# Kernel tuning notes

Measured on AMD Instinct MI355X. Metric: run time of the kernel, lower is better.

Reference implementation:

```python
import jax, jax.numpy as jnp
import numpy as np

N = 20000
F_IN = 128
HID = 128
HEADS = 8
NCLS = 18
NEG_SLOPE = 0.2


def setup_inputs() -> dict:
    key = jax.random.key(0)
    ks = jax.random.split(key, 12)
    x = jax.random.normal(ks[0], (N, F_IN), dtype=jnp.float32)
    edge_index = jax.random.randint(ks[1], (2, 200000), 0, N)
    sc1 = 1.0 / np.sqrt(F_IN)
    sc2 = 1.0 / np.sqrt(HEADS * HID)
    W1 = jax.random.normal(ks[2], (F_IN, HEADS * HID), dtype=jnp.float32) * sc1
    a1_src = jax.random.normal(ks[3], (HEADS, HID), dtype=jnp.float32) * sc1
    a1_dst = jax.random.normal(ks[4], (HEADS, HID), dtype=jnp.float32) * sc1
    b1 = jnp.zeros((HEADS * HID,), dtype=jnp.float32)
    W2 = jax.random.normal(ks[5], (HEADS * HID, NCLS), dtype=jnp.float32) * sc2
    a2_src = jax.random.normal(ks[6], (1, NCLS), dtype=jnp.float32) * sc2
    a2_dst = jax.random.normal(ks[7], (1, NCLS), dtype=jnp.float32) * sc2
    b2 = jnp.zeros((NCLS,), dtype=jnp.float32)
    return {"x": x, "edge_index": edge_index, "W1": W1, "a1_src": a1_src,
            "a1_dst": a1_dst, "b1": b1, "W2": W2, "a2_src": a2_src,
            "a2_dst": a2_dst, "b2": b2}


def gat_conv(x, src, dst, W, a_src, a_dst, b, heads, out_ch):
    n = x.shape[0]
    h = (x @ W).reshape(n, heads, out_ch)              # [N,H,C]
    alpha_s = jnp.sum(h * a_src, axis=-1)              # [N,H]
    alpha_d = jnp.sum(h * a_dst, axis=-1)              # [N,H]
    e = jax.nn.leaky_relu(alpha_s[src] + alpha_d[dst], NEG_SLOPE)  # [E,H]
    # per-destination softmax (segment softmax)
    m = jax.ops.segment_max(e, dst, num_segments=n)
    e = jnp.exp(e - m[dst])
    z = jax.ops.segment_sum(e, dst, num_segments=n)
    alpha = e / (z[dst] + 1e-16)                       # [E,H]
    out = jax.ops.segment_sum(alpha[:, :, None] * h[src], dst, num_segments=n)
    return out.reshape(n, heads * out_ch) + b


def reference(x, edge_index, W1, a1_src, a1_dst, b1, W2, a2_src, a2_dst, b2):
    n = x.shape[0]
    # PyG GATConv adds self-loops by default
    loops = jnp.arange(n, dtype=edge_index.dtype)
    src = jnp.concatenate([edge_index[0], loops])
    dst = jnp.concatenate([edge_index[1], loops])
    h = gat_conv(x, src, dst, W1, a1_src, a1_dst, b1, HEADS, HID)
    h = jax.nn.relu(h)
    # F.dropout(training=self.training) is identity in eval mode
    out = gat_conv(h, src, dst, W2, a2_src, a2_dst, b2, 1, NCLS)
    return out
```

## Files before the change

kernel.cpp:

```cpp
#include <hip/hip_runtime.h>
#include <math.h>

#define FIN 128
#define NH 8
#define HC 128
#define HD (NH*HC)
#define NC 18
#define NW2 32
#define NEG 0.2f

typedef __attribute__((ext_vector_type(8))) short bf16x8;
typedef __attribute__((ext_vector_type(4))) float f32x4;

__device__ __forceinline__ float lrelu(float v){ return v > 0.f ? v : NEG*v; }

__device__ __forceinline__ unsigned short f2b(float f){
  unsigned u = __float_as_uint(f);
  unsigned r = (u + 0x7fffu + ((u >> 16) & 1u)) >> 16;
  return (unsigned short)r;
}
__device__ __forceinline__ float b2f_lo(unsigned u){ return __uint_as_float(u << 16); }
__device__ __forceinline__ float b2f_hi(unsigned u){ return __uint_as_float(u & 0xffff0000u); }

__device__ __forceinline__ void acc8(float* a, float w, uint4 r){
  a[0] += w*b2f_lo(r.x); a[1] += w*b2f_hi(r.x);
  a[2] += w*b2f_lo(r.y); a[3] += w*b2f_hi(r.y);
  a[4] += w*b2f_lo(r.z); a[5] += w*b2f_hi(r.z);
  a[6] += w*b2f_lo(r.w); a[7] += w*b2f_hi(r.w);
}

__global__ __launch_bounds__(1024) void scan_k(const int* __restrict__ deg, int N,
                                               int* __restrict__ off, int* __restrict__ cursor){
  __shared__ int wsum[16];
  int t = threadIdx.x, lane = t & 63, wid = t >> 6;
  int PER = (N + 1023) >> 10;
  int base = t * PER;
  int sum = 0;
  for (int i = 0; i < PER; ++i) {
    int idx = base + i;
    if (idx < N) sum += deg[idx];
  }
  int x = sum;
  #pragma unroll
  for (int o = 1; o < 64; o <<= 1) {
    int y = __shfl_up(x, o, 64);
    if (lane >= o) x += y;
  }
  if (lane == 63) wsum[wid] = x;
  __syncthreads();
  if (wid == 0 && lane < 16) {
    int wv = wsum[lane];
    #pragma unroll
    for (int o = 1; o < 16; o <<= 1) {
      int y = __shfl_up(wv, o, 16);
      if (lane >= o) wv += y;
    }
    wsum[lane] = wv;
  }
  __syncthreads();
  int carry = x - sum + (wid > 0 ? wsum[wid-1] : 0);
  int run = carry;
  for (int i = 0; i < PER; ++i) {
    int idx = base + i;
    if (idx < N) {
      off[idx] = run; cursor[idx] = run;
      run += deg[idx];
    }
  }
  if (base < N && base + PER >= N) off[N] = run;
}

__global__ void scatter_k(const int* __restrict__ ei, int E0, int N,
                          int* __restrict__ cursor, int* __restrict__ csr){
  int e = blockIdx.x*256 + threadIdx.x;
  int tot = E0 + N;
  if (e >= tot) return;
  int src, dst;
  if (e < E0) { src = ei[e]; dst = ei[E0 + e]; }
  else        { src = e - E0; dst = src; }
  int p = atomicAdd(&cursor[dst], 1);
  csr[p] = src;
}

__global__ __launch_bounds__(256) void prep_k(const float* __restrict__ x,
    const float* __restrict__ W1, const float* __restrict__ W2,
    const float* __restrict__ a1s, const float* __restrict__ a1d,
    const int* __restrict__ ei,
    unsigned short* __restrict__ xb, unsigned short* __restrict__ w1t,
    unsigned short* __restrict__ w2t, unsigned short* __restrict__ ut_g,
    int* __restrict__ deg,
    int total8, int bX, int E0, int N){
  __shared__ unsigned short sT[FIN][64+2];
  int b = blockIdx.x, t = threadIdx.x;
  if (b < bX) {
    int i = b*256 + t;
    if (i < total8) {
      const float4* p = (const float4*)x + (size_t)i*2;
      float4 a = p[0], c = p[1];
      uint4 o;
      o.x = (unsigned)f2b(a.x) | ((unsigned)f2b(a.y) << 16);
      o.y = (unsigned)f2b(a.z) | ((unsigned)f2b(a.w) << 16);
      o.z = (unsigned)f2b(c.x) | ((unsigned)f2b(c.y) << 16);
      o.w = (unsigned)f2b(c.z) | ((unsigned)f2b(c.w) << 16);
      ((uint4*)xb)[i] = o;
    }
    return;
  }
  b -= bX;
  if (b < 16) {
    int n0 = b * 64;
    #pragma unroll
    for (int i = 0; i < 32; ++i) {
      int idx = i*256 + t;
      int k = idx >> 6, nl = idx & 63;
      sT[k][nl] = f2b(W1[(size_t)k*HD + n0 + nl]);
    }
    __syncthreads();
    #pragma unroll
    for (int i = 0; i < 16; ++i) {
      int nl = i*4 + (t >> 6);
      int kp = t & 63;
      unsigned u = (unsigned)sT[2*kp][nl] | ((unsigned)sT[2*kp+1][nl] << 16);
      *(unsigned*)&w1t[(size_t)(n0+nl)*FIN + 2*kp] = u;
    }
    return;
  }
  b -= 16;
  if (b < (NW2*HD)/256) {
    int idx = b*256 + t;
    int n = idx >> 10, k = idx & 1023;
    w2t[idx] = (n < NC) ? f2b(W2[(size_t)k*NC + n]) : (unsigned short)0;
    return;
  }
  b -= (NW2*HD)/256;
  if (b < 16) {
    int c = b;
    int h = c >> 1;
    const float* av = (c & 1) ? &a1d[h*HC] : &a1s[h*HC];
    if (t < FIN) {
      const float4* wr = (const float4*)&W1[(size_t)t*HD + h*HC];
      const float4* ap = (const float4*)av;
      float s = 0.f;
      #pragma unroll 8
      for (int q = 0; q < HC/4; ++q) {
        float4 w4 = wr[q], a4 = ap[q];
        s += w4.x*a4.x + w4.y*a4.y + w4.z*a4.z + w4.w*a4.w;
      }
      ut_g[c*FIN + t] = f2b(s);
    }
    return;
  }
  b -= 16;
  {
    int e = b*256 + t;
    int tot = E0 + N;
    if (e >= tot) return;
    int dst = (e < E0) ? ei[E0 + e] : (e - E0);
    atomicAdd(&deg[dst], 1);
  }
}

__global__ __launch_bounds__(256) void gemm1_mfma_k(const unsigned short* __restrict__ xb,
    const unsigned short* __restrict__ w1t, const unsigned short* __restrict__ ut_g,
    unsigned short* __restrict__ g1b, float* __restrict__ as1, float* __restrict__ ad1,
    int N){
  __shared__ unsigned short sA[128][136];
  __shared__ unsigned short sB[128][136];
  __shared__ unsigned short sU[16][136];
  int t = threadIdx.x, lane = t & 63, wid = t >> 6;
  int bm = blockIdx.x * 128;
  int head = blockIdx.y;
  int bn = head * 128;
  #pragma unroll
  for (int i = 0; i < 2; ++i) {
    int idx = i*256 + t;
    int row = idx >> 2, seg = idx & 3;
    int gm = bm + row;
    uint4 a0,a1,a2,a3;
    if (gm < N) {
      const uint4* gp = (const uint4*)(xb + (size_t)gm*FIN + seg*32);
      a0 = gp[0]; a1 = gp[1]; a2 = gp[2]; a3 = gp[3];
    } else {
      a0 = a1 = a2 = a3 = make_uint4(0,0,0,0);
    }
    uint4* lp = (uint4*)&sA[row][seg*32];
    lp[0]=a0; lp[1]=a1; lp[2]=a2; lp[3]=a3;
  }
  #pragma unroll
  for (int i = 0; i < 2; ++i) {
    int idx = i*256 + t;
    int row = idx >> 2, seg = idx & 3;
    const uint4* gp = (const uint4*)(w1t + (size_t)(bn + row)*FIN + seg*32);
    uint4* lp = (uint4*)&sB[row][seg*32];
    lp[0]=gp[0]; lp[1]=gp[1]; lp[2]=gp[2]; lp[3]=gp[3];
  }
  bool alpha_blk = (head == 0);
  if (alpha_blk) {
    int row = t >> 4, seg = t & 15;
    *(uint4*)&sU[row][seg*8] = *(const uint4*)&ut_g[row*FIN + seg*8];
  }
  __syncthreads();
  int wr = wid >> 1, wc = wid & 1;
  int lr = lane & 15, kb = lane >> 4;
  bool alpha_wave = alpha_blk && (wc == 0);
  f32x4 acc[4][4];
  f32x4 accA[4];
  #pragma unroll
  for (int mi = 0; mi < 4; ++mi) {
    f32x4 z = {0.f,0.f,0.f,0.f};
    accA[mi] = z;
    #pragma unroll
    for (int ni = 0; ni < 4; ++ni) acc[mi][ni] = z;
  }
  #pragma unroll
  for (int ks = 0; ks < 4; ++ks) {
    int ko = ks*32 + kb*8;
    bf16x8 a[4], b[4];
    #pragma unroll
    for (int mi = 0; mi < 4; ++mi)
      a[mi] = *(const bf16x8*)&sA[wr*64 + mi*16 + lr][ko];
    #pragma unroll
    for (int ni = 0; ni < 4; ++ni)
      b[ni] = *(const bf16x8*)&sB[wc*64 + ni*16 + lr][ko];
    #pragma unroll
    for (int mi = 0; mi < 4; ++mi)
      #pragma unroll
      for (int ni = 0; ni < 4; ++ni)
        acc[mi][ni] = __builtin_amdgcn_mfma_f32_16x16x32_bf16(a[mi], b[ni], acc[mi][ni], 0, 0, 0);
    if (alpha_wave) {
      bf16x8 ub = *(const bf16x8*)&sU[lr][ko];
      #pragma unroll
      for (int mi = 0; mi < 4; ++mi)
        accA[mi] = __builtin_amdgcn_mfma_f32_16x16x32_bf16(a[mi], ub, accA[mi], 0, 0, 0);
    }
  }
  __syncthreads();

  if (alpha_wave) {
    int hcol = lr >> 1;
    float* dst0 = (lr & 1) ? ad1 : as1;
    #pragma unroll
    for (int mi = 0; mi < 4; ++mi)
      #pragma unroll
      for (int r = 0; r < 4; ++r) {
        int row = bm + wr*64 + mi*16 + kb*4 + r;
        if (row < N) dst0[(size_t)row*NH + hcol] = accA[mi][r];
      }
  }
  #pragma unroll
  for (int mi = 0; mi < 4; ++mi)
    #pragma unroll
    for (int ni = 0; ni < 4; ++ni) {
      int col = wc*64 + ni*16 + lr;
      #pragma unroll
      for (int r = 0; r < 4; ++r)
        sA[wr*64 + mi*16 + kb*4 + r][col] = f2b(acc[mi][ni][r]);
    }
  __syncthreads();
  {
    int row = t >> 1, half = t & 1;
    int grow = bm + row;
    if (grow < N) {
      uint4* dst = (uint4*)(g1b + (size_t)grow*HD + bn + half*64);
      const uint4* src = (const uint4*)&sA[row][half*64];
      #pragma unroll
      for (int q = 0; q < 8; ++q) dst[q] = src[q];
    }
  }
}

__global__ __launch_bounds__(256) void attn1_k(const unsigned short* __restrict__ g1b,
    const float* __restrict__ as1, const float* __restrict__ ad1,
    const int* __restrict__ off, const int* __restrict__ csr,
    const float* __restrict__ b1, const unsigned short* __restrict__ w2t,
    const float* __restrict__ a2s_g, const float* __restrict__ a2d_g,
    float* __restrict__ g2, float* __restrict__ as2, float* __restrict__ ad2, int N){
  __shared__ unsigned short tile[16][1032];
  __shared__ float red[4][4][32];
  int t = threadIdx.x, lane = t & 63, wid = t >> 6;
  int d = blockIdx.x*4 + wid;
  bool active = (d < N);
  int beg = 0, deg = 0;
  int hg = lane >> 3;
  float adg = 0.f;
  if (active) {
    beg = off[d]; deg = off[d+1] - beg;
    adg = ad1[d*NH + hg];
  }
  float m = -1e30f, z = 0.f;
  float acc[16];
  #pragma unroll
  for (int i = 0; i < 16; ++i) acc[i] = 0.f;

  int j = 0;
  for (; j + 4 <= deg; j += 4) {
    int s0 = csr[beg+j+0], s1 = csr[beg+j+1], s2 = csr[beg+j+2], s3 = csr[beg+j+3];
    const uint4* p0 = (const uint4*)(g1b + (size_t)s0*HD) + lane*2;
    const uint4* p1 = (const uint4*)(g1b + (size_t)s1*HD) + lane*2;
    const uint4* p2 = (const uint4*)(g1b + (size_t)s2*HD) + lane*2;
    const uint4* p3 = (const uint4*)(g1b + (size_t)s3*HD) + lane*2;
    uint4 r00 = p0[0], r01 = p0[1];
    uint4 r10 = p1[0], r11 = p1[1];
    uint4 r20 = p2[0], r21 = p2[1];
    uint4 r30 = p3[0], r31 = p3[1];
    float e0 = lrelu(as1[s0*NH+hg] + adg);
    float e1 = lrelu(as1[s1*NH+hg] + adg);
    float e2 = lrelu(as1[s2*NH+hg] + adg);
    float e3 = lrelu(as1[s3*NH+hg] + adg);
    float em = fmaxf(fmaxf(e0,e1), fmaxf(e2,e3));
    if (em > m) {
      float sc = __expf(m - em);
      z *= sc;
      #pragma unroll
      for (int i = 0; i < 16; ++i) acc[i] *= sc;
      m = em;
    }
    float w0 = __expf(e0 - m), w1 = __expf(e1 - m);
    float w2 = __expf(e2 - m), w3 = __expf(e3 - m);
    z += w0 + w1 + w2 + w3;
    acc8(acc, w0, r00); acc8(acc+8, w0, r01);
    acc8(acc, w1, r10); acc8(acc+8, w1, r11);
    acc8(acc, w2, r20); acc8(acc+8, w2, r21);
    acc8(acc, w3, r30); acc8(acc+8, w3, r31);
  }
  for (; j < deg; ++j) {
    int s = csr[beg+j];
    const uint4* p = (const uint4*)(g1b + (size_t)s*HD) + lane*2;
    uint4 r0 = p[0], r1 = p[1];
    float e = lrelu(as1[s*NH+hg] + adg);
    if (e > m) {
      float sc = __expf(m - e);
      z *= sc;
      #pragma unroll
      for (int i = 0; i < 16; ++i) acc[i] *= sc;
      m = e;
    }
    float w = __expf(e - m);
    z += w;
    acc8(acc, w, r0); acc8(acc+8, w, r1);
  }

  {
    float zinv = 1.f / (z + 1e-16f);
    int cb = lane*16;
    uint o[8];
    #pragma unroll
    for (int q = 0; q < 4; ++q) {
      float4 bv = *(const float4*)&b1[cb + q*4];
      float v0 = fmaxf(acc[q*4+0]*zinv + bv.x, 0.f);
      float v1 = fmaxf(acc[q*4+1]*zinv + bv.y, 0.f);
      float v2 = fmaxf(acc[q*4+2]*zinv + bv.z, 0.f);
      float v3 = fmaxf(acc[q*4+3]*zinv + bv.w, 0.f);
      o[q*2+0] = (unsigned)f2b(v0) | ((unsigned)f2b(v1) << 16);
      o[q*2+1] = (unsigned)f2b(v2) | ((unsigned)f2b(v3) << 16);
    }
    uint4* lp = (uint4*)&tile[wid][lane*16];
    lp[0] = make_uint4(o[0], o[1], o[2], o[3]);
    lp[1] = make_uint4(o[4], o[5], o[6], o[7]);
  }
  __syncthreads();

  {
    int lr = lane & 15, kb = lane >> 4;
    f32x4 c0 = {0.f,0.f,0.f,0.f}, c1 = {0.f,0.f,0.f,0.f};
    #pragma unroll
    for (int ks = 0; ks < 8; ++ks) {
      int k = wid*256 + ks*32 + kb*8;
      bf16x8 af = *(const bf16x8*)&tile[lr][k];
      bf16x8 b0 = *(const bf16x8*)&w2t[(size_t)lr*HD + k];
      bf16x8 b1f = *(const bf16x8*)&w2t[(size_t)(16+lr)*HD + k];
      c0 = __builtin_amdgcn_mfma_f32_16x16x32_bf16(af, b0, c0, 0,0,0);
      c1 = __builtin_amdgcn_mfma_f32_16x16x32_bf16(af, b1f, c1, 0,0,0);
    }
    if (kb == 0) {
      #pragma unroll
      for (int r = 0; r < 4; ++r) {
        red[wid][r][lr]      = c0[r];
        red[wid][r][16 + lr] = c1[r];
      }
    }
  }
  __syncthreads();
  if (t < 128) {
    int dl = t >> 5, c = t & 31;
    float v = red[0][dl][c] + red[1][dl][c] + red[2][dl][c] + red[3][dl][c];
    float vs = (c < NC) ? v * a2s_g[c] : 0.f;
    float vd = (c < NC) ? v * a2d_g[c] : 0.f;
    #pragma unroll
    for (int o = 1; o < 32; o <<= 1) {
      vs += __shfl_xor(vs, o, 32);
      vd += __shfl_xor(vd, o, 32);
    }
    int dg = blockIdx.x*4 + dl;
    if (dg < N) {
      if (c < NC) g2[(size_t)dg*NC + c] = v;
      if (c == 0) { as2[dg] = vs; ad2[dg] = vd; }
    }
  }
}

__global__ __launch_bounds__(256) void attn2_k(const float* __restrict__ g2,
    const float* __restrict__ as2, const float* __restrict__ ad2,
    const int* __restrict__ off, const int* __restrict__ csr,
    const float* __restrict__ b2, float* __restrict__ out, int N){
  int t = threadIdx.x, lane = t & 63, wid = t >> 6;
  int d = blockIdx.x*4 + wid;
  if (d >= N) return;
  int beg = off[d], deg = off[d+1] - beg;
  float adv = ad2[d];
  int g = lane / 18;
  int c = lane - g*18;
  float m = -1e30f, z = 0.f, acc = 0.f;
  if (g < 3) {
    int j = g;
    for (; j + 3 < deg; j += 6) {
      int sa = csr[beg+j], sb = csr[beg+j+3];
      float va = g2[(size_t)sa*NC + c];
      float vb = g2[(size_t)sb*NC + c];
      float ea = lrelu(as2[sa] + adv);
      float eb = lrelu(as2[sb] + adv);
      float em = fmaxf(ea, eb);
      if (em > m) { float sc = __expf(m - em); z *= sc; acc *= sc; m = em; }
      float wa = __expf(ea - m), wb = __expf(eb - m);
      z += wa + wb;
      acc += wa*va + wb*vb;
    }
    for (; j < deg; j += 3) {
      int s = csr[beg+j];
      float v = g2[(size_t)s*NC + c];
      float e = lrelu(as2[s] + adv);
      if (e > m) { float sc = __expf(m - e); z *= sc; acc *= sc; m = e; }
      float w = __expf(e - m);
      z += w;
      acc += w*v;
    }
  }
  float m0 = __shfl(m, 0),  m1 = __shfl(m, 18), m2 = __shfl(m, 36);
  float M  = fmaxf(m0, fmaxf(m1, m2));
  float e0 = __expf(m0 - M), e1 = __expf(m1 - M), e2 = __expf(m2 - M);
  float z0 = __shfl(z, 0),  z1 = __shfl(z, 18), z2 = __shfl(z, 36);
  int cl = (lane < NC) ? lane : 0;
  float a0 = __shfl(acc, cl), a1 = __shfl(acc, cl+18), a2 = __shfl(acc, cl+36);
  if (lane < NC) {
    float Z = z0*e0 + z1*e1 + z2*e2;
    float A = a0*e0 + a1*e1 + a2*e2;
    out[(size_t)d*NC + lane] = A / (Z + 1e-16f) + b2[lane];
  }
}

extern "C" void kernel_launch(void* const* d_in, const int* in_sizes, int n_in,
                              void* d_out, int out_size, void* d_ws, size_t ws_size,
                              hipStream_t stream){
  const float* x   = (const float*)d_in[0];
  const int*   ei  = (const int*)d_in[1];
  const float* W1  = (const float*)d_in[2];
  const float* a1s = (const float*)d_in[3];
  const float* a1d = (const float*)d_in[4];
  const float* b1  = (const float*)d_in[5];
  const float* W2  = (const float*)d_in[6];
  const float* a2s = (const float*)d_in[7];
  const float* a2d = (const float*)d_in[8];
  const float* b2  = (const float*)d_in[9];
  float* out = (float*)d_out;
  int N  = in_sizes[0] / FIN;
  int E0 = in_sizes[1] / 2;
  int Etot = E0 + N;

  float* as1 = (float*)d_ws;
  float* ad1 = as1 + (size_t)N*NH;
  float* g2  = ad1 + (size_t)N*NH;
  float* as2 = g2 + (size_t)N*NC;
  float* ad2 = as2 + N;
  unsigned short* g1b  = (unsigned short*)(ad2 + N);
  unsigned short* scr  = g1b + (size_t)N*HD;
  int* deg    = (int*)(scr + (size_t)N*HD);
  int* off    = deg + N;
  int* cursor = off + N + 4;
  int* csr    = cursor + N;
  unsigned short* w2t  = (unsigned short*)(csr + Etot);
  unsigned short* ut_g = w2t + (size_t)NW2*HD;
  unsigned short* xb  = scr;
  unsigned short* w1t = scr + (size_t)N*FIN;

  hipMemsetAsync(deg, 0, sizeof(int)*(size_t)N, stream);

  int total8 = N*FIN/8;
  int bX = (total8 + 255)/256;
  int bH = (Etot + 255)/256;
  int bW2 = (NW2*HD)/256;
  prep_k<<<bX + 16 + bW2 + 16 + bH, 256, 0, stream>>>(x, W1, W2, a1s, a1d, ei,
                                                      xb, w1t, w2t, ut_g, deg,
                                                      total8, bX, E0, N);
  scan_k<<<1, 1024, 0, stream>>>(deg, N, off, cursor);
  scatter_k<<<(Etot+255)/256, 256, 0, stream>>>(ei, E0, N, cursor, csr);

  dim3 g1grid((N+127)/128, HD/128);
  gemm1_mfma_k<<<g1grid, 256, 0, stream>>>(xb, w1t, ut_g, g1b, as1, ad1, N);
  attn1_k<<<(N+3)/4, 256, 0, stream>>>(g1b, as1, ad1, off, csr, b1, w2t,
                                       a2s, a2d, g2, as2, ad2, N);
  attn2_k<<<(N+3)/4, 256, 0, stream>>>(g2, as2, ad2, off, csr, b2, out, N);
}
```

Before: 259.4 us.

## Replace MFMA second-layer projection with per-wave dot products and shuffle reduction

Measured after the change: 265.8 us. 2.5% more time.

```diff
diff --git a/kernel.cpp b/kernel.cpp
--- a/kernel.cpp
+++ b/kernel.cpp
@@ -275,18 +275,21 @@
     const float* __restrict__ b1, const unsigned short* __restrict__ w2t,
     const float* __restrict__ a2s_g, const float* __restrict__ a2d_g,
     float* __restrict__ g2, float* __restrict__ as2, float* __restrict__ ad2, int N){
-  __shared__ unsigned short tile[16][1032];
-  __shared__ float red[4][4][32];
+  __shared__ unsigned short sW2[NC][1024];
   int t = threadIdx.x, lane = t & 63, wid = t >> 6;
+  {
+    const uint4* src = (const uint4*)w2t;
+    uint4* dst = (uint4*)&sW2[0][0];
+    #pragma unroll
+    for (int i = 0; i < (NC*1024)/8/256; ++i)
+      dst[i*256 + t] = src[i*256 + t];
+  }
+  __syncthreads();
   int d = blockIdx.x*4 + wid;
-  bool active = (d < N);
-  int beg = 0, deg = 0;
+  if (d >= N) return;
+  int beg = off[d], deg = off[d+1] - beg;
   int hg = lane >> 3;
-  float adg = 0.f;
-  if (active) {
-    beg = off[d]; deg = off[d+1] - beg;
-    adg = ad1[d*NH + hg];
-  }
+  float adg = ad1[d*NH + hg];
   float m = -1e30f, z = 0.f;
   float acc[16];
   #pragma unroll
@@ -340,62 +343,49 @@
     acc8(acc, w, r0); acc8(acc+8, w, r1);
   }
 
-  {
-    float zinv = 1.f / (z + 1e-16f);
-    int cb = lane*16;
-    uint o[8];
-    #pragma unroll
-    for (int q = 0; q < 4; ++q) {
-      float4 bv = *(const float4*)&b1[cb + q*4];
-      float v0 = fmaxf(acc[q*4+0]*zinv + bv.x, 0.f);
-      float v1 = fmaxf(acc[q*4+1]*zinv + bv.y, 0.f);
-      float v2 = fmaxf(acc[q*4+2]*zinv + bv.z, 0.f);
-      float v3 = fmaxf(acc[q*4+3]*zinv + bv.w, 0.f);
-      o[q*2+0] = (unsigned)f2b(v0) | ((unsigned)f2b(v1) << 16);
-      o[q*2+1] = (unsigned)f2b(v2) | ((unsigned)f2b(v3) << 16);
-    }
-    uint4* lp = (uint4*)&tile[wid][lane*16];
-    lp[0] = make_uint4(o[0], o[1], o[2], o[3]);
-    lp[1] = make_uint4(o[4], o[5], o[6], o[7]);
-  }
-  __syncthreads();
-
-  {
-    int lr = lane & 15, kb = lane >> 4;
-    f32x4 c0 = {0.f,0.f,0.f,0.f}, c1 = {0.f,0.f,0.f,0.f};
-    #pragma unroll
-    for (int ks = 0; ks < 8; ++ks) {
-      int k = wid*256 + ks*32 + kb*8;
-      bf16x8 af = *(const bf16x8*)&tile[lr][k];
-      bf16x8 b0 = *(const bf16x8*)&w2t[(size_t)lr*HD + k];
-      bf16x8 b1f = *(const bf16x8*)&w2t[(size_t)(16+lr)*HD + k];
-      c0 = __builtin_amdgcn_mfma_f32_16x16x32_bf16(af, b0, c0, 0,0,0);
-      c1 = __builtin_amdgcn_mfma_f32_16x16x32_bf16(af, b1f, c1, 0,0,0);
-    }
-    if (kb == 0) {
-      #pragma unroll
-      for (int r = 0; r < 4; ++r) {
-        red[wid][r][lr]      = c0[r];
-        red[wid][r][16 + lr] = c1[r];
-      }
-    }
-  }
-  __syncthreads();
-  if (t < 128) {
-    int dl = t >> 5, c = t & 31;
-    float v = red[0][dl][c] + red[1][dl][c] + red[2][dl][c] + red[3][dl][c];
-    float vs = (c < NC) ? v * a2s_g[c] : 0.f;
-    float vd = (c < NC) ? v * a2d_g[c] : 0.f;
-    #pragma unroll
-    for (int o = 1; o < 32; o <<= 1) {
-      vs += __shfl_xor(vs, o, 32);
-      vd += __shfl_xor(vd, o, 32);
-    }
-    int dg = blockIdx.x*4 + dl;
-    if (dg < N) {
-      if (c < NC) g2[(size_t)dg*NC + c] = v;
-      if (c == 0) { as2[dg] = vs; ad2[dg] = vd; }
-    }
+  float zinv = 1.f / (z + 1e-16f);
+  int cb = lane*16;
+  float h[16];
+  #pragma unroll
+  for (int q = 0; q < 4; ++q) {
+    float4 bv = *(const float4*)&b1[cb + q*4];
+    h[q*4+0] = fmaxf(acc[q*4+0]*zinv + bv.x, 0.f);
+    h[q*4+1] = fmaxf(acc[q*4+1]*zinv + bv.y, 0.f);
+    h[q*4+2] = fmaxf(acc[q*4+2]*zinv + bv.z, 0.f);
+    h[q*4+3] = fmaxf(acc[q*4+3]*zinv + bv.w, 0.f);
+  }
+
+  float part[NC];
+  #pragma unroll
+  for (int c = 0; c < NC; ++c) {
+    const uint4* wp = (const uint4*)&sW2[c][cb];
+    uint4 u0 = wp[0], u1 = wp[1];
+    float s;
+    s  = h[ 0]*b2f_lo(u0.x) + h[ 1]*b2f_hi(u0.x);
+    s += h[ 2]*b2f_lo(u0.y) + h[ 3]*b2f_hi(u0.y);
+    s += h[ 4]*b2f_lo(u0.z) + h[ 5]*b2f_hi(u0.z);
+    s += h[ 6]*b2f_lo(u0.w) + h[ 7]*b2f_hi(u0.w);
+    s += h[ 8]*b2f_lo(u1.x) + h[ 9]*b2f_hi(u1.x);
+    s += h[10]*b2f_lo(u1.y) + h[11]*b2f_hi(u1.y);
+    s += h[12]*b2f_lo(u1.z) + h[13]*b2f_hi(u1.z);
+    s += h[14]*b2f_lo(u1.w) + h[15]*b2f_hi(u1.w);
+    part[c] = s;
+  }
+  #pragma unroll
+  for (int o = 1; o < 64; o <<= 1) {
+    #pragma unroll
+    for (int c = 0; c < NC; ++c)
+      part[c] += __shfl_xor(part[c], o, 64);
+  }
+  if (lane == 0) {
+    float s = 0.f, dd = 0.f;
+    #pragma unroll
+    for (int c = 0; c < NC; ++c) {
+      g2[(size_t)d*NC + c] = part[c];
+      s  += part[c]*a2s_g[c];
+      dd += part[c]*a2d_g[c];
+    }
+    as2[d] = s; ad2[d] = dd;
   }
 }
 
@@ -471,8 +461,8 @@
   float* g2  = ad1 + (size_t)N*NH;
   float* as2 = g2 + (size_t)N*NC;
   float* ad2 = as2 + N;
-  unsigned short* g1b  = (unsigned short*)(ad2 + N);
-  unsigned short* scr  = g1b + (size_t)N*HD;
+  unsigned short* g1b = (unsigned short*)(ad2 + N);
+  unsigned short* scr = g1b + (size_t)N*HD;
   int* deg    = (int*)(scr + (size_t)N*HD);
   int* off    = deg + N;
   int* cursor = off + N + 4;
```
